# Kernel optimization log

Measured on AMD Instinct MI355X. Metric: run time of the kernel, lower is better.

Reference implementation:

```python
import jax, jax.numpy as jnp
import numpy as np

B, N, D = 2, 1024, 1024
H, DH = 16, 64          # nhead, head_dim (D = H*DH)
FF = 4096               # dim_feedforward = 4*D
E = 8                   # num experts
EPS = 1e-5


def layer_norm(x, s, b):
    m = jnp.mean(x, -1, keepdims=True)
    v = jnp.mean((x - m) ** 2, -1, keepdims=True)
    return (x - m) * jax.lax.rsqrt(v + EPS) * s + b


def moe_gate(x, Wg):
    # top-1 gating: expert index + gate probability per token
    probs = jax.nn.softmax(x @ Wg, axis=-1)            # [B,N,E]
    idx = jnp.argmax(probs, axis=-1)                   # [B,N]
    gw = jnp.take_along_axis(probs, idx[..., None], -1)[..., 0]  # [B,N]
    return idx, gw


def moe_linear(x, W, b, idx, gw):
    # x:[B,N,Din], W:[E,Din,Dout], b:[E,Dout]; route each token to expert idx
    y = jnp.einsum('bnd,edh->bneh', x, W) + b          # [B,N,E,Dout]
    oh = jax.nn.one_hot(idx, E, dtype=x.dtype)         # [B,N,E]
    return jnp.einsum('bneh,bne->bnh', y, oh) * gw[..., None]


def setup_inputs() -> dict:
    key = jax.random.key(0)
    ks = jax.random.split(key, 8)
    g = lambda k, shape, sc: jax.random.normal(k, shape, jnp.float32) * sc
    inv_d = 1.0 / np.sqrt(D)
    return dict(
        src=g(ks[0], (B, N, D), 1.0),
        key_padding_mask=jnp.zeros((B, N), dtype=bool),
        Wg_attn=g(ks[1], (D, E), inv_d),
        Wqkv=g(ks[2], (E, D, 3 * D), inv_d), bqkv=jnp.zeros((E, 3 * D), jnp.float32),
        Wo=g(ks[3], (E, D, D), inv_d), bo=jnp.zeros((E, D), jnp.float32),
        Wg_ffn=g(ks[4], (D, E), inv_d),
        W1=g(ks[5], (E, D, FF), inv_d), b1=jnp.zeros((E, FF), jnp.float32),
        W2=g(ks[6], (E, FF, D), 1.0 / np.sqrt(FF)), b2=jnp.zeros((E, D), jnp.float32),
        ln1_s=jnp.ones((D,), jnp.float32), ln1_b=jnp.zeros((D,), jnp.float32),
        ln2_s=jnp.ones((D,), jnp.float32), ln2_b=jnp.zeros((D,), jnp.float32),
    )


def reference(src, key_padding_mask, Wg_attn, Wqkv, bqkv, Wo, bo,
              Wg_ffn, W1, b1, W2, b2, ln1_s, ln1_b, ln2_s, ln2_b):
    # attention mask: key_padding_mask.unsqueeze(1).unsqueeze(1) * -10000
    mask = jnp.where(key_padding_mask[:, None, None, :], -10000.0, 0.0).astype(src.dtype)

    # --- MoE self-attention (gate decided once, reused for qkv and dense) ---
    idx, gw = moe_gate(src, Wg_attn)
    qkv = moe_linear(src, Wqkv, bqkv, idx, gw)                 # [B,N,3D]
    q, k, v = jnp.split(qkv, 3, axis=-1)
    heads = lambda t: t.reshape(B, N, H, DH).transpose(0, 2, 1, 3)  # [B,H,N,DH]
    q, k, v = heads(q), heads(k), heads(v)
    scores = jnp.einsum('bhqd,bhkd->bhqk', q, k) / np.sqrt(DH) + mask
    probs = jax.nn.softmax(scores, axis=-1)
    ctx = jnp.einsum('bhqk,bhkd->bhqd', probs, v)
    ctx = ctx.transpose(0, 2, 1, 3).reshape(B, N, D)
    attn_out = moe_linear(ctx, Wo, bo, idx, gw)

    # post-norm residual
    x = layer_norm(src + attn_out, ln1_s, ln1_b)

    # --- MoE FFN (its own gate, shared across both linears) ---
    fidx, fgw = moe_gate(x, Wg_ffn)
    h = jax.nn.gelu(moe_linear(x, W1, b1, fidx, fgw))
    ffn = moe_linear(h, W2, b2, fidx, fgw)

    return layer_norm(x + ffn, ln2_s, ln2_b)
```

## Files before the change

kernel.cpp:

```cpp
#include <hip/hip_runtime.h>


#define B_   2
#define N_   1024
#define D_   1024
#define H_   16
#define DH_  64
#define FF_  4096
#define E_   8
#define NTOK 2048

typedef __attribute__((ext_vector_type(8))) short short8;
typedef __attribute__((ext_vector_type(8))) unsigned short ushort8;
typedef __attribute__((ext_vector_type(4))) unsigned short ushort4v;
typedef __attribute__((ext_vector_type(4))) float f32x4;

__device__ inline unsigned short f2bf(float f) {
  unsigned u = __float_as_uint(f);
  u += 0x7FFFu + ((u >> 16) & 1u);
  return (unsigned short)(u >> 16);
}

__device__ inline float gelu_tanh(float x) {
  float x3 = x * x * x;
  float t = tanhf(0.7978845608028654f * (x + 0.044715f * x3));
  return 0.5f * x * (1.0f + t);
}

__global__ __launch_bounds__(256) void gate_kernel(
    const float* __restrict__ X, const float* __restrict__ Wg,
    int* __restrict__ idx, float* __restrict__ gwv, int* __restrict__ cnt) {
  int t = blockIdx.x * 4 + (threadIdx.x >> 6);
  int lane = threadIdx.x & 63;
  const float* x = X + (size_t)t * D_;
  float acc[E_];
#pragma unroll
  for (int j = 0; j < E_; j++) acc[j] = 0.f;
#pragma unroll
  for (int i = 0; i < 16; i++) {
    int d = i * 64 + lane;
    float xv = x[d];
    const float4* w = (const float4*)(Wg + (size_t)d * E_);
    float4 w0 = w[0], w1 = w[1];
    acc[0] += xv * w0.x; acc[1] += xv * w0.y; acc[2] += xv * w0.z; acc[3] += xv * w0.w;
    acc[4] += xv * w1.x; acc[5] += xv * w1.y; acc[6] += xv * w1.z; acc[7] += xv * w1.w;
  }
#pragma unroll
  for (int o = 1; o < 64; o <<= 1) {
#pragma unroll
    for (int j = 0; j < E_; j++) acc[j] += __shfl_xor(acc[j], o, 64);
  }
  float m = acc[0]; int bi = 0;
#pragma unroll
  for (int j = 1; j < E_; j++) { if (acc[j] > m) { m = acc[j]; bi = j; } }
  float den = 0.f;
#pragma unroll
  for (int j = 0; j < E_; j++) den += expf(acc[j] - m);
  float gw = expf(acc[bi] - m) / den;
  if (lane == 0) { idx[t] = bi; gwv[t] = gw; atomicAdd(&cnt[bi], 1); }
}

__global__ __launch_bounds__(256) void route_kernel(
    const int* __restrict__ idx, const int* __restrict__ cnt,
    int* __restrict__ off, int* __restrict__ perm, int ntok) {
  __shared__ int loff[E_ + 1];
  __shared__ int lfill[E_];
  if (threadIdx.x == 0) {
    int s = 0;
    for (int e = 0; e < E_; e++) { loff[e] = s; s += cnt[e]; }
    loff[E_] = s;
  }
  if (threadIdx.x < E_) lfill[threadIdx.x] = 0;
  __syncthreads();
  for (int t = (int)threadIdx.x; t < ntok; t += 256) {
    int e = idx[t];
    int p = atomicAdd(&lfill[e], 1);
    perm[loff[e] + p] = t;
  }
  if (threadIdx.x < E_ + 1) off[threadIdx.x] = loff[threadIdx.x];
}

template <typename AT, int KS>
__global__ __launch_bounds__(512, 2) void gemm_kernel(
    const AT* __restrict__ A, int ldA,
    const float* __restrict__ W,
    const int* __restrict__ perm, const int* __restrict__ off,
    float* __restrict__ part, int K, int N) {
  __shared__ __align__(16) unsigned short As[256][40];
  __shared__ __align__(16) unsigned short Bs[128][40];
  __shared__ int toks[256];

  int e = blockIdx.y;
  int base = off[e];
  int cnt = off[e + 1] - base;
  int mt = blockIdx.z / KS;
  int kc = blockIdx.z % KS;
  int m0 = mt * 256;
  if (m0 >= cnt) return;
  int rows_valid = min(256, cnt - m0);
  int tid = threadIdx.x;
  if (tid < 256) {
    int r = (tid < rows_valid) ? tid : (rows_valid - 1);
    toks[tid] = perm[base + m0 + r];
  }
  int nb = blockIdx.x * 128;
  int lane = tid & 63, wave = tid >> 6;
  int wm = (wave & 3) * 64, wn = (wave >> 2) * 64;
  int lr = lane & 15, lg = lane >> 4;
  f32x4 acc[4][4];
#pragma unroll
  for (int m = 0; m < 4; m++)
#pragma unroll
    for (int n = 0; n < 4; n++) acc[m][n] = (f32x4){0.f, 0.f, 0.f, 0.f};
  int srow = tid >> 1, koff = (tid & 1) * 16;
  int k2 = (tid & 15) * 2, cB = tid >> 4;
  int n0 = cB * 4;
  int KL = K / KS;
  int kbeg = kc * KL;
  __syncthreads();

  for (int k0 = kbeg; k0 < kbeg + KL; k0 += 32) {
    {
      const AT* ar = A + (size_t)toks[srow] * ldA + k0 + koff;
      ushort8 o0, o1;
      if constexpr (sizeof(AT) == 4) {
        const float* fa = (const float*)ar;
        float4 v0 = *(const float4*)(fa);
        float4 v1 = *(const float4*)(fa + 4);
        float4 v2 = *(const float4*)(fa + 8);
        float4 v3 = *(const float4*)(fa + 12);
        o0[0] = f2bf(v0.x); o0[1] = f2bf(v0.y); o0[2] = f2bf(v0.z); o0[3] = f2bf(v0.w);
        o0[4] = f2bf(v1.x); o0[5] = f2bf(v1.y); o0[6] = f2bf(v1.z); o0[7] = f2bf(v1.w);
        o1[0] = f2bf(v2.x); o1[1] = f2bf(v2.y); o1[2] = f2bf(v2.z); o1[3] = f2bf(v2.w);
        o1[4] = f2bf(v3.x); o1[5] = f2bf(v3.y); o1[6] = f2bf(v3.z); o1[7] = f2bf(v3.w);
      } else {
        o0 = *(const ushort8*)ar;
        o1 = *(const ushort8*)(ar + 8);
      }
      *(ushort8*)&As[srow][koff] = o0;
      *(ushort8*)&As[srow][koff + 8] = o1;
    }
    {
      const float* w0 = W + ((size_t)e * K + k0 + k2) * N + nb + n0;
      float4 r0 = *(const float4*)w0;
      float4 r1 = *(const float4*)(w0 + N);
      float lo[4] = {r0.x, r0.y, r0.z, r0.w};
      float hi[4] = {r1.x, r1.y, r1.z, r1.w};
#pragma unroll
      for (int j = 0; j < 4; j++) {
        int n = n0 + j;
        int sc = (((k2 >> 3) ^ ((n >> 2) & 3)) << 3) | (k2 & 7);
        unsigned v = (unsigned)f2bf(lo[j]) | ((unsigned)f2bf(hi[j]) << 16);
        *(unsigned*)&Bs[n][sc] = v;
      }
    }
    __syncthreads();
    short8 av[4], bv[4];
#pragma unroll
    for (int m = 0; m < 4; m++) av[m] = *(const short8*)&As[wm + m * 16 + lr][lg * 8];
#pragma unroll
    for (int n = 0; n < 4; n++) {
      int nn = wn + n * 16 + lr;
      int blk = lg ^ ((nn >> 2) & 3);
      bv[n] = *(const short8*)&Bs[nn][blk * 8];
    }
#pragma unroll
    for (int m = 0; m < 4; m++)
#pragma unroll
      for (int n = 0; n < 4; n++)
        acc[m][n] = __builtin_amdgcn_mfma_f32_16x16x32_bf16(av[m], bv[n], acc[m][n], 0, 0, 0);
    __syncthreads();
  }

  float* pr = part + (size_t)kc * ((size_t)NTOK * N);
#pragma unroll
  for (int n = 0; n < 4; n++) {
    int col = nb + wn + n * 16 + lr;
#pragma unroll
    for (int m = 0; m < 4; m++) {
#pragma unroll
      for (int reg = 0; reg < 4; reg++) {
        int r = wm + m * 16 + lg * 4 + reg;
        if (r < rows_valid)
          pr[(size_t)toks[r] * N + col] = acc[m][n][reg];
      }
    }
  }
}

template <int KS, bool GELU, bool OBF16>
__global__ __launch_bounds__(256) void reduce_kernel(
    const float* __restrict__ part, const float* __restrict__ bias,
    const float* __restrict__ gwv, const int* __restrict__ idx,
    void* __restrict__ out, int N) {
  int t = blockIdx.y;
  int n = (blockIdx.x * 256 + threadIdx.x) * 4;
  int e = idx[t];
  float gw = gwv[t];
  const float* p = part + (size_t)t * N + n;
  float4 a = *(const float4*)p;
#pragma unroll
  for (int k = 1; k < KS; k++) {
    float4 q = *(const float4*)(p + (size_t)k * NTOK * N);
    a.x += q.x; a.y += q.y; a.z += q.z; a.w += q.w;
  }
  float4 bv = *(const float4*)(bias + (size_t)e * N + n);
  a.x = (a.x + bv.x) * gw; a.y = (a.y + bv.y) * gw;
  a.z = (a.z + bv.z) * gw; a.w = (a.w + bv.w) * gw;
  if constexpr (GELU) {
    a.x = gelu_tanh(a.x); a.y = gelu_tanh(a.y);
    a.z = gelu_tanh(a.z); a.w = gelu_tanh(a.w);
  }
  if constexpr (OBF16) {
    ushort4v o;
    o[0] = f2bf(a.x); o[1] = f2bf(a.y); o[2] = f2bf(a.z); o[3] = f2bf(a.w);
    *(ushort4v*)((unsigned short*)out + (size_t)t * N + n) = o;
  } else {
    *(float4*)((float*)out + (size_t)t * N + n) = a;
  }
}

__global__ __launch_bounds__(256) void vtrans_kernel(
    const unsigned short* __restrict__ qkv, unsigned short* __restrict__ vT) {
  __shared__ __align__(16) unsigned short T[64][72];
  int bh = blockIdx.x;
  int b = bh >> 4, h = bh & 15;
  int tile = blockIdx.y;
  int tid = threadIdx.x;
  {
    int tk = tid >> 2, dof = (tid & 3) * 16;
    const unsigned short* p =
        qkv + ((size_t)(b * N_ + tile * 64 + tk)) * 3072 + 2048 + h * 64 + dof;
    *(ushort8*)&T[tk][dof] = *(const ushort8*)p;
    *(ushort8*)&T[tk][dof + 8] = *(const ushort8*)(p + 8);
  }
  __syncthreads();
  {
    int dh = tid >> 2, tof = (tid & 3) * 16;
    ushort8 o0, o1;
#pragma unroll
    for (int i = 0; i < 8; i++) o0[i] = T[tof + i][dh];
#pragma unroll
    for (int i = 0; i < 8; i++) o1[i] = T[tof + 8 + i][dh];
    unsigned short* q = vT + ((size_t)bh * 64 + dh) * N_ + tile * 64 + tof;
    *(ushort8*)q = o0;
    *(ushort8*)(q + 8) = o1;
  }
}

__global__ __launch_bounds__(256) void attn_kernel(
    const unsigned short* __restrict__ qkv, const unsigned short* __restrict__ vT,
    const unsigned char* __restrict__ kpm, unsigned short* __restrict__ ctx) {
  __shared__ __align__(16) unsigned short Qs[64][72];
  __shared__ __align__(16) unsigned short Ks[64][72];
  __shared__ __align__(16) unsigned short Vs[64][72];
  __shared__ __align__(16) unsigned short Ps[4][16][72];
  __shared__ float maskf[64];
  int qt = blockIdx.x, bh = blockIdx.y;
  int b = bh >> 4, h = bh & 15;
  int tid = threadIdx.x, lane = tid & 63, wave = tid >> 6;
  int lr = lane & 15, lg = lane >> 4;
  {
    int r = tid >> 2, dof = (tid & 3) * 16;
    const unsigned short* p = qkv + ((size_t)(b * N_ + qt * 64 + r)) * 3072 + h * 64 + dof;
    *(ushort8*)&Qs[r][dof] = *(const ushort8*)p;
    *(ushort8*)&Qs[r][dof + 8] = *(const ushort8*)(p + 8);
  }
  __syncthreads();
  short8 aq[2];
  aq[0] = *(const short8*)&Qs[wave * 16 + lr][lg * 8];
  aq[1] = *(const short8*)&Qs[wave * 16 + lr][32 + lg * 8];
  f32x4 O[4];
  float mrun[4], lrun[4];
#pragma unroll
  for (int r = 0; r < 4; r++) { mrun[r] = -1e30f; lrun[r] = 0.f; O[r] = (f32x4){0.f, 0.f, 0.f, 0.f}; }

  for (int kt = 0; kt < 16; kt++) {
    __syncthreads();
    {
      int r = tid >> 2, dof = (tid & 3) * 16;
      const unsigned short* p =
          qkv + ((size_t)(b * N_ + kt * 64 + r)) * 3072 + 1024 + h * 64 + dof;
      *(ushort8*)&Ks[r][dof] = *(const ushort8*)p;
      *(ushort8*)&Ks[r][dof + 8] = *(const ushort8*)(p + 8);
      const unsigned short* pv = vT + ((size_t)bh * 64 + r) * N_ + kt * 64 + dof;
      *(ushort8*)&Vs[r][dof] = *(const ushort8*)pv;
      *(ushort8*)&Vs[r][dof + 8] = *(const ushort8*)(pv + 8);
      if (tid < 64) maskf[tid] = kpm[b * N_ + kt * 64 + tid] ? -10000.f : 0.f;
    }
    __syncthreads();
    f32x4 S[4];
#pragma unroll
    for (int n = 0; n < 4; n++) {
      f32x4 s = (f32x4){0.f, 0.f, 0.f, 0.f};
#pragma unroll
      for (int ks = 0; ks < 2; ks++) {
        short8 bk = *(const short8*)&Ks[n * 16 + lr][ks * 32 + lg * 8];
        s = __builtin_amdgcn_mfma_f32_16x16x32_bf16(aq[ks], bk, s, 0, 0, 0);
      }
      float mv = maskf[n * 16 + lr];
#pragma unroll
      for (int r = 0; r < 4; r++) s[r] = s[r] * 0.125f + mv;
      S[n] = s;
    }
    float cur[4];
#pragma unroll
    for (int r = 0; r < 4; r++)
      cur[r] = fmaxf(fmaxf(S[0][r], S[1][r]), fmaxf(S[2][r], S[3][r]));
#pragma unroll
    for (int o = 1; o < 16; o <<= 1) {
#pragma unroll
      for (int r = 0; r < 4; r++) cur[r] = fmaxf(cur[r], __shfl_xor(cur[r], o, 64));
    }
    float alpha[4], rsum[4];
#pragma unroll
    for (int r = 0; r < 4; r++) {
      float mn = fmaxf(mrun[r], cur[r]);
      alpha[r] = expf(mrun[r] - mn);
      mrun[r] = mn;
      rsum[r] = 0.f;
    }
#pragma unroll
    for (int n = 0; n < 4; n++) {
#pragma unroll
      for (int r = 0; r < 4; r++) {
        S[n][r] = expf(S[n][r] - mrun[r]);
        rsum[r] += S[n][r];
      }
    }
#pragma unroll
    for (int o = 1; o < 16; o <<= 1) {
#pragma unroll
      for (int r = 0; r < 4; r++) rsum[r] += __shfl_xor(rsum[r], o, 64);
    }
#pragma unroll
    for (int r = 0; r < 4; r++) lrun[r] = lrun[r] * alpha[r] + rsum[r];
#pragma unroll
    for (int d = 0; d < 4; d++)
#pragma unroll
      for (int r = 0; r < 4; r++) O[d][r] *= alpha[r];
#pragma unroll
    for (int n = 0; n < 4; n++)
#pragma unroll
      for (int r = 0; r < 4; r++) Ps[wave][lg * 4 + r][n * 16 + lr] = f2bf(S[n][r]);
    short8 pf[2];
    pf[0] = *(const short8*)&Ps[wave][lr][lg * 8];
    pf[1] = *(const short8*)&Ps[wave][lr][32 + lg * 8];
#pragma unroll
    for (int d = 0; d < 4; d++) {
#pragma unroll
      for (int ks = 0; ks < 2; ks++) {
        short8 bv = *(const short8*)&Vs[d * 16 + lr][ks * 32 + lg * 8];
        O[d] = __builtin_amdgcn_mfma_f32_16x16x32_bf16(pf[ks], bv, O[d], 0, 0, 0);
      }
    }
  }
#pragma unroll
  for (int r = 0; r < 4; r++) lrun[r] = 1.f / lrun[r];
#pragma unroll
  for (int d = 0; d < 4; d++) {
#pragma unroll
    for (int r = 0; r < 4; r++) {
      int q = qt * 64 + wave * 16 + lg * 4 + r;
      int dh = d * 16 + lr;
      ctx[((size_t)(b * N_ + q)) * D_ + h * DH_ + dh] = f2bf(O[d][r] * lrun[r]);
    }
  }
}

template <int KS>
__global__ __launch_bounds__(256) void ln_reduce_kernel(
    const float* __restrict__ res, const float* __restrict__ part,
    const float* __restrict__ bias, const float* __restrict__ gwv,
    const int* __restrict__ idx,
    const float* __restrict__ S, const float* __restrict__ Bi,
    float* __restrict__ O) {
  int t = blockIdx.x, tid = threadIdx.x;
  int e = idx[t];
  float gw = gwv[t];
  const float* p = part + (size_t)t * D_ + tid * 4;
  float4 a = *(const float4*)p;
#pragma unroll
  for (int k = 1; k < KS; k++) {
    float4 q = *(const float4*)(p + (size_t)k * NTOK * D_);
    a.x += q.x; a.y += q.y; a.z += q.z; a.w += q.w;
  }
  float4 bv4 = *(const float4*)(bias + (size_t)e * D_ + tid * 4);
  float4 vr = ((const float4*)(res + (size_t)t * D_))[tid];
  float4 v;
  v.x = vr.x + (a.x + bv4.x) * gw;
  v.y = vr.y + (a.y + bv4.y) * gw;
  v.z = vr.z + (a.z + bv4.z) * gw;
  v.w = vr.w + (a.w + bv4.w) * gw;
  float s = v.x + v.y + v.z + v.w;
  float sq = v.x * v.x + v.y * v.y + v.z * v.z + v.w * v.w;
#pragma unroll
  for (int o = 1; o < 64; o <<= 1) {
    s += __shfl_xor(s, o, 64);
    sq += __shfl_xor(sq, o, 64);
  }
  __shared__ float ss[4], ssq[4];
  int wave = tid >> 6, lane = tid & 63;
  if (lane == 0) { ss[wave] = s; ssq[wave] = sq; }
  __syncthreads();
  float ts = ss[0] + ss[1] + ss[2] + ss[3];
  float tsq = ssq[0] + ssq[1] + ssq[2] + ssq[3];
  float mean = ts * (1.f / D_);
  float var = tsq * (1.f / D_) - mean * mean;
  float rs = rsqrtf(var + 1e-5f);
  float4 sv = ((const float4*)S)[tid];
  float4 bi = ((const float4*)Bi)[tid];
  float4 o;
  o.x = (v.x - mean) * rs * sv.x + bi.x;
  o.y = (v.y - mean) * rs * sv.y + bi.y;
  o.z = (v.z - mean) * rs * sv.z + bi.z;
  o.w = (v.w - mean) * rs * sv.w + bi.w;
  ((float4*)(O + (size_t)t * D_))[tid] = o;
}

extern "C" void kernel_launch(void* const* d_in, const int* in_sizes, int n_in,
                              void* d_out, int out_size, void* d_ws, size_t ws_size,
                              hipStream_t stream) {
  (void)in_sizes; (void)n_in; (void)out_size; (void)ws_size;
  const float* src     = (const float*)d_in[0];
  const unsigned char* kpm = (const unsigned char*)d_in[1];
  const float* Wg_attn = (const float*)d_in[2];
  const float* Wqkv    = (const float*)d_in[3];
  const float* bqkv    = (const float*)d_in[4];
  const float* Wo      = (const float*)d_in[5];
  const float* bo      = (const float*)d_in[6];
  const float* Wg_ffn  = (const float*)d_in[7];
  const float* W1      = (const float*)d_in[8];
  const float* b1      = (const float*)d_in[9];
  const float* W2      = (const float*)d_in[10];
  const float* b2      = (const float*)d_in[11];
  const float* ln1_s   = (const float*)d_in[12];
  const float* ln1_b   = (const float*)d_in[13];
  const float* ln2_s   = (const float*)d_in[14];
  const float* ln2_b   = (const float*)d_in[15];
  float* out = (float*)d_out;

  char* ws = (char*)d_ws;
  size_t o = 0;
  auto alloc = [&](size_t bytes) -> void* {
    void* p = ws + o;
    o += (bytes + 255) & ~(size_t)255;
    return p;
  };
  int* meta = (int*)alloc(256);
  int* cnt1 = meta;
  int* off1 = meta + 8;
  int* cnt2 = meta + 17;
  int* off2 = meta + 25;
  int* idx1 = (int*)alloc(NTOK * 4);
  float* gw1 = (float*)alloc(NTOK * 4);
  int* perm1 = (int*)alloc(NTOK * 4);
  int* idx2 = (int*)alloc(NTOK * 4);
  float* gw2 = (float*)alloc(NTOK * 4);
  int* perm2 = (int*)alloc(NTOK * 4);
  unsigned short* qkvb = (unsigned short*)alloc((size_t)NTOK * 3072 * 2);
  unsigned short* vT = (unsigned short*)alloc((size_t)32 * 64 * N_ * 2);
  unsigned short* hbuf = qkvb;
  unsigned short* ctx = (unsigned short*)alloc((size_t)NTOK * D_ * 2);
  float* x = (float*)alloc((size_t)NTOK * D_ * 4);
  float* part = (float*)alloc((size_t)2 * NTOK * FF_ * 4);

  hipMemsetAsync(meta, 0, 256, stream);

  gate_kernel<<<512, 256, 0, stream>>>(src, Wg_attn, idx1, gw1, cnt1);
  route_kernel<<<1, 256, 0, stream>>>(idx1, cnt1, off1, perm1, NTOK);
  gemm_kernel<float, 2><<<dim3(3072 / 128, 8, 16), 512, 0, stream>>>(
      src, 1024, Wqkv, perm1, off1, part, 1024, 3072);
  reduce_kernel<2, false, true><<<dim3(3, NTOK), 256, 0, stream>>>(
      part, bqkv, gw1, idx1, qkvb, 3072);
  vtrans_kernel<<<dim3(32, 16), 256, 0, stream>>>(qkvb, vT);
  attn_kernel<<<dim3(16, 32), 256, 0, stream>>>(qkvb, vT, kpm, ctx);
  gemm_kernel<unsigned short, 4><<<dim3(1024 / 128, 8, 32), 512, 0, stream>>>(
      ctx, 1024, Wo, perm1, off1, part, 1024, 1024);
  ln_reduce_kernel<4><<<NTOK, 256, 0, stream>>>(
      src, part, bo, gw1, idx1, ln1_s, ln1_b, x);

  gate_kernel<<<512, 256, 0, stream>>>(x, Wg_ffn, idx2, gw2, cnt2);
  route_kernel<<<1, 256, 0, stream>>>(idx2, cnt2, off2, perm2, NTOK);
  gemm_kernel<float, 2><<<dim3(4096 / 128, 8, 16), 512, 0, stream>>>(
      x, 1024, W1, perm2, off2, part, 1024, 4096);
  reduce_kernel<2, true, true><<<dim3(4, NTOK), 256, 0, stream>>>(
      part, b1, gw2, idx2, hbuf, 4096);
  gemm_kernel<unsigned short, 4><<<dim3(1024 / 128, 8, 32), 512, 0, stream>>>(
      hbuf, 4096, W2, perm2, off2, part, 4096, 1024);
  ln_reduce_kernel<4><<<NTOK, 256, 0, stream>>>(
      x, part, b2, gw2, idx2, ln2_s, ln2_b, out);
}
```

Baseline: 696.1 us.

## Pre-cast GEMM activations to bf16 and double-buffer A tiles via direct LDS loads

```diff
diff --git a/kernel.cpp b/kernel.cpp
--- a/kernel.cpp
+++ b/kernel.cpp
@@ -80,13 +80,24 @@
   if (threadIdx.x < E_ + 1) off[threadIdx.x] = loff[threadIdx.x];
 }
 
-template <typename AT, int KS>
-__global__ __launch_bounds__(512, 2) void gemm_kernel(
-    const AT* __restrict__ A, int ldA,
+__global__ __launch_bounds__(256) void cast_bf16_kernel(
+    const float* __restrict__ in, unsigned short* __restrict__ out) {
+  size_t i = ((size_t)blockIdx.x * 256 + threadIdx.x) * 8;
+  float4 v0 = *(const float4*)(in + i);
+  float4 v1 = *(const float4*)(in + i + 4);
+  ushort8 o;
+  o[0] = f2bf(v0.x); o[1] = f2bf(v0.y); o[2] = f2bf(v0.z); o[3] = f2bf(v0.w);
+  o[4] = f2bf(v1.x); o[5] = f2bf(v1.y); o[6] = f2bf(v1.z); o[7] = f2bf(v1.w);
+  *(ushort8*)(out + i) = o;
+}
+
+template <int KS>
+__global__ __launch_bounds__(512, 4) void gemm_kernel(
+    const unsigned short* __restrict__ A, int ldA,
     const float* __restrict__ W,
     const int* __restrict__ perm, const int* __restrict__ off,
     float* __restrict__ part, int K, int N) {
-  __shared__ __align__(16) unsigned short As[256][40];
+  __shared__ __align__(16) unsigned short As[2][256][32];
   __shared__ __align__(16) unsigned short Bs[128][40];
   __shared__ int toks[256];
 
@@ -112,64 +123,77 @@
   for (int m = 0; m < 4; m++)
 #pragma unroll
     for (int n = 0; n < 4; n++) acc[m][n] = (f32x4){0.f, 0.f, 0.f, 0.f};
-  int srow = tid >> 1, koff = (tid & 1) * 16;
-  int k2 = (tid & 15) * 2, cB = tid >> 4;
-  int n0 = cB * 4;
-  int KL = K / KS;
-  int kbeg = kc * KL;
+
+  int a_rowl = lane >> 2, a_j = lane & 3;
+  int ar0 = wave * 32 + a_rowl;
+  int kb2 = (tid & 15) * 2, n0 = (tid >> 4) * 4;
+
+  int KL = K / KS, kbeg = kc * KL, kend = kbeg + KL;
   __syncthreads();
 
-  for (int k0 = kbeg; k0 < kbeg + KL; k0 += 32) {
+  float4 r0, r1;
+  {
+#pragma unroll
+    for (int i = 0; i < 2; i++) {
+      int row = ar0 + i * 16;
+      int s = (row >> 1) & 3;
+      const unsigned short* g = A + (size_t)toks[row] * ldA + kbeg + ((a_j ^ s) << 3);
+      __builtin_amdgcn_global_load_lds(
+          (const __attribute__((address_space(1))) unsigned int*)g,
+          (__attribute__((address_space(3))) unsigned int*)&As[0][wave * 32 + i * 16][0],
+          16, 0, 0);
+    }
+    const float* w0 = W + ((size_t)e * K + kbeg + kb2) * N + nb + n0;
+    r0 = *(const float4*)w0;
+    r1 = *(const float4*)(w0 + N);
+  }
+
+  int buf = 0;
+  for (int k0 = kbeg; k0 < kend; k0 += 32) {
     {
-      const AT* ar = A + (size_t)toks[srow] * ldA + k0 + koff;
-      ushort8 o0, o1;
-      if constexpr (sizeof(AT) == 4) {
-        const float* fa = (const float*)ar;
-        float4 v0 = *(const float4*)(fa);
-        float4 v1 = *(const float4*)(fa + 4);
-        float4 v2 = *(const float4*)(fa + 8);
-        float4 v3 = *(const float4*)(fa + 12);
-        o0[0] = f2bf(v0.x); o0[1] = f2bf(v0.y); o0[2] = f2bf(v0.z); o0[3] = f2bf(v0.w);
-        o0[4] = f2bf(v1.x); o0[5] = f2bf(v1.y); o0[6] = f2bf(v1.z); o0[7] = f2bf(v1.w);
-        o1[0] = f2bf(v2.x); o1[1] = f2bf(v2.y); o1[2] = f2bf(v2.z); o1[3] = f2bf(v2.w);
-        o1[4] = f2bf(v3.x); o1[5] = f2bf(v3.y); o1[6] = f2bf(v3.z); o1[7] = f2bf(v3.w);
-      } else {
-        o0 = *(const ushort8*)ar;
-        o1 = *(const ushort8*)(ar + 8);
-      }
-      *(ushort8*)&As[srow][koff] = o0;
-      *(ushort8*)&As[srow][koff + 8] = o1;
-    }
-    {
-      const float* w0 = W + ((size_t)e * K + k0 + k2) * N + nb + n0;
-      float4 r0 = *(const float4*)w0;
-      float4 r1 = *(const float4*)(w0 + N);
       float lo[4] = {r0.x, r0.y, r0.z, r0.w};
       float hi[4] = {r1.x, r1.y, r1.z, r1.w};
 #pragma unroll
       for (int j = 0; j < 4; j++) {
         int n = n0 + j;
-        int sc = (((k2 >> 3) ^ ((n >> 2) & 3)) << 3) | (k2 & 7);
+        int sc = (((kb2 >> 3) ^ ((n >> 2) & 3)) << 3) | (kb2 & 7);
         unsigned v = (unsigned)f2bf(lo[j]) | ((unsigned)f2bf(hi[j]) << 16);
         *(unsigned*)&Bs[n][sc] = v;
       }
     }
     __syncthreads();
-    short8 av[4], bv[4];
-#pragma unroll
-    for (int m = 0; m < 4; m++) av[m] = *(const short8*)&As[wm + m * 16 + lr][lg * 8];
+    if (k0 + 32 < kend) {
+      int kn = k0 + 32;
+#pragma unroll
+      for (int i = 0; i < 2; i++) {
+        int row = ar0 + i * 16;
+        int s = (row >> 1) & 3;
+        const unsigned short* g = A + (size_t)toks[row] * ldA + kn + ((a_j ^ s) << 3);
+        __builtin_amdgcn_global_load_lds(
+            (const __attribute__((address_space(1))) unsigned int*)g,
+            (__attribute__((address_space(3))) unsigned int*)&As[buf ^ 1][wave * 32 + i * 16][0],
+            16, 0, 0);
+      }
+      const float* w0 = W + ((size_t)e * K + kn + kb2) * N + nb + n0;
+      r0 = *(const float4*)w0;
+      r1 = *(const float4*)(w0 + N);
+    }
+    short8 av[4];
+#pragma unroll
+    for (int m = 0; m < 4; m++) {
+      int r = wm + m * 16 + lr;
+      av[m] = *(const short8*)&As[buf][r][(lg ^ ((r >> 1) & 3)) << 3];
+    }
 #pragma unroll
     for (int n = 0; n < 4; n++) {
       int nn = wn + n * 16 + lr;
-      int blk = lg ^ ((nn >> 2) & 3);
-      bv[n] = *(const short8*)&Bs[nn][blk * 8];
-    }
-#pragma unroll
-    for (int m = 0; m < 4; m++)
-#pragma unroll
-      for (int n = 0; n < 4; n++)
-        acc[m][n] = __builtin_amdgcn_mfma_f32_16x16x32_bf16(av[m], bv[n], acc[m][n], 0, 0, 0);
+      short8 bv = *(const short8*)&Bs[nn][(lg ^ ((nn >> 2) & 3)) << 3];
+#pragma unroll
+      for (int m = 0; m < 4; m++)
+        acc[m][n] = __builtin_amdgcn_mfma_f32_16x16x32_bf16(av[m], bv, acc[m][n], 0, 0, 0);
+    }
     __syncthreads();
+    buf ^= 1;
   }
 
   float* pr = part + (size_t)kc * ((size_t)NTOK * N);
@@ -368,13 +392,13 @@
   }
 }
 
-template <int KS>
+template <int KS, bool WBF>
 __global__ __launch_bounds__(256) void ln_reduce_kernel(
     const float* __restrict__ res, const float* __restrict__ part,
     const float* __restrict__ bias, const float* __restrict__ gwv,
     const int* __restrict__ idx,
     const float* __restrict__ S, const float* __restrict__ Bi,
-    float* __restrict__ O) {
+    float* __restrict__ O, unsigned short* __restrict__ Obf) {
   int t = blockIdx.x, tid = threadIdx.x;
   int e = idx[t];
   float gw = gwv[t];
@@ -416,6 +440,11 @@
   o.z = (v.z - mean) * rs * sv.z + bi.z;
   o.w = (v.w - mean) * rs * sv.w + bi.w;
   ((float4*)(O + (size_t)t * D_))[tid] = o;
+  if constexpr (WBF) {
+    ushort4v ob;
+    ob[0] = f2bf(o.x); ob[1] = f2bf(o.y); ob[2] = f2bf(o.z); ob[3] = f2bf(o.w);
+    *(ushort4v*)(Obf + (size_t)t * D_ + tid * 4) = ob;
+  }
 }
 
 extern "C" void kernel_launch(void* const* d_in, const int* in_sizes, int n_in,
@@ -462,32 +491,35 @@
   unsigned short* vT = (unsigned short*)alloc((size_t)32 * 64 * N_ * 2);
   unsigned short* hbuf = qkvb;
   unsigned short* ctx = (unsigned short*)alloc((size_t)NTOK * D_ * 2);
+  unsigned short* src_bf = ctx;
+  unsigned short* x_bf = ctx;
   float* x = (float*)alloc((size_t)NTOK * D_ * 4);
   float* part = (float*)alloc((size_t)2 * NTOK * FF_ * 4);
 
   hipMemsetAsync(meta, 0, 256, stream);
 
+  cast_bf16_kernel<<<1024, 256, 0, stream>>>(src, src_bf);
   gate_kernel<<<512, 256, 0, stream>>>(src, Wg_attn, idx1, gw1, cnt1);
   route_kernel<<<1, 256, 0, stream>>>(idx1, cnt1, off1, perm1, NTOK);
-  gemm_kernel<float, 2><<<dim3(3072 / 128, 8, 16), 512, 0, stream>>>(
-      src, 1024, Wqkv, perm1, off1, part, 1024, 3072);
+  gemm_kernel<2><<<dim3(3072 / 128, 8, 16), 512, 0, stream>>>(
+      src_bf, 1024, Wqkv, perm1, off1, part, 1024, 3072);
   reduce_kernel<2, false, true><<<dim3(3, NTOK), 256, 0, stream>>>(
       part, bqkv, gw1, idx1, qkvb, 3072);
   vtrans_kernel<<<dim3(32, 16), 256, 0, stream>>>(qkvb, vT);
   attn_kernel<<<dim3(16, 32), 256, 0, stream>>>(qkvb, vT, kpm, ctx);
-  gemm_kernel<unsigned short, 4><<<dim3(1024 / 128, 8, 32), 512, 0, stream>>>(
+  gemm_kernel<4><<<dim3(1024 / 128, 8, 32), 512, 0, stream>>>(
       ctx, 1024, Wo, perm1, off1, part, 1024, 1024);
-  ln_reduce_kernel<4><<<NTOK, 256, 0, stream>>>(
-      src, part, bo, gw1, idx1, ln1_s, ln1_b, x);
+  ln_reduce_kernel<4, true><<<NTOK, 256, 0, stream>>>(
+      src, part, bo, gw1, idx1, ln1_s, ln1_b, x, x_bf);
 
   gate_kernel<<<512, 256, 0, stream>>>(x, Wg_ffn, idx2, gw2, cnt2);
   route_kernel<<<1, 256, 0, stream>>>(idx2, cnt2, off2, perm2, NTOK);
-  gemm_kernel<float, 2><<<dim3(4096 / 128, 8, 16), 512, 0, stream>>>(
-      x, 1024, W1, perm2, off2, part, 1024, 4096);
+  gemm_kernel<2><<<dim3(4096 / 128, 8, 16), 512, 0, stream>>>(
+      x_bf, 1024, W1, perm2, off2, part, 1024, 4096);
   reduce_kernel<2, true, true><<<dim3(4, NTOK), 256, 0, stream>>>(
       part, b1, gw2, idx2, hbuf, 4096);
-  gemm_kernel<unsigned short, 4><<<dim3(1024 / 128, 8, 32), 512, 0, stream>>>(
+  gemm_kernel<4><<<dim3(1024 / 128, 8, 32), 512, 0, stream>>>(
       hbuf, 4096, W2, perm2, off2, part, 4096, 1024);
-  ln_reduce_kernel<4><<<NTOK, 256, 0, stream>>>(
-      x, part, b2, gw2, idx2, ln2_s, ln2_b, out);
-}
+  ln_reduce_kernel<4, false><<<NTOK, 256, 0, stream>>>(
+      x, part, b2, gw2, idx2, ln2_s, ln2_b, out, (unsigned short*)nullptr);
+}
```

New measurement: 672.4 us. 1.04x faster.
